# Optimization experiments

Hardware: AMD Instinct MI355X
Metric: run time of the kernel (lower is better)

Reference implementation:

```python
import jax, jax.numpy as jnp
import numpy as np
from functools import partial

PERPLEXITY = 30.0
TOL = 1e-05
K = int(3 * PERPLEXITY)  # neighbors kept after dropping self
N_CAT = 8
N_TRIES = 50


def setup_inputs() -> dict:
    key = jax.random.key(0)
    k1, k2 = jax.random.split(key)
    x = jax.random.normal(k1, (8192, 64), dtype=jnp.float32)
    batch_id = jax.random.randint(k2, (8192,), 0, N_CAT, dtype=jnp.int32)
    return {"x": x, "batch_id": batch_id}


def _knn(x):
    # squared Euclidean pairwise distances [N, N]
    sq = jnp.sum(x * x, axis=-1)
    d2 = sq[:, None] + sq[None, :] - 2.0 * (x @ x.T)
    d2 = jnp.maximum(d2, 0.0)
    neg, idx = jax.lax.top_k(-d2, K + 1)  # nearest K+1 incl. self
    dist = jnp.sqrt(jnp.maximum(-neg[:, 1:], 0.0))  # drop self -> [N, K] Euclidean
    return dist, idx[:, 1:]


def _hbeta(dist, beta):
    # dist: [N, K], beta: [N] -> entropy H [N], normalized P [N, K]
    P = jnp.exp(-dist * beta[:, None])
    Psum = jnp.sum(P, axis=1)
    safe = Psum > 0
    Psafe = jnp.where(safe, Psum, 1.0)
    H = jnp.where(safe, jnp.log(Psafe) + beta * jnp.sum(dist * P, axis=1) / Psafe, 0.0)
    Pn = jnp.where(safe[:, None], P / Psafe[:, None], 0.0)
    return H, Pn


def _beta_search(dist):
    N = dist.shape[0]
    logU = jnp.log(jnp.float32(PERPLEXITY))
    beta = jnp.ones((N,), dist.dtype)
    bmin = jnp.full((N,), -jnp.inf, dist.dtype)
    bmax = jnp.full((N,), jnp.inf, dist.dtype)
    H, P = _hbeta(dist, beta)
    Hdiff = H - logU

    def step(carry, _):
        beta, bmin, bmax, H, P, Hdiff = carry
        done = jnp.abs(Hdiff) < TOL
        pos = Hdiff > 0
        nbmin = jnp.where(pos, beta, bmin)
        nbmax = jnp.where(pos, bmax, beta)
        b_up = jnp.where(jnp.isfinite(bmax), (beta + bmax) * 0.5, beta * 2.0)
        b_dn = jnp.where(jnp.isfinite(bmin), (beta + bmin) * 0.5, beta * 0.5)
        nbeta = jnp.where(pos, b_up, b_dn)
        beta2 = jnp.where(done, beta, nbeta)
        bmin2 = jnp.where(done, bmin, nbmin)
        bmax2 = jnp.where(done, bmax, nbmax)
        Hn, Pn = _hbeta(dist, beta2)
        H2 = jnp.where(done, H, Hn)
        P2 = jnp.where(done[:, None], P, Pn)
        return (beta2, bmin2, bmax2, H2, P2, H2 - logU), None

    (beta, bmin, bmax, H, P, Hdiff), _ = jax.lax.scan(
        step, (beta, bmin, bmax, H, P, Hdiff), None, length=N_TRIES)
    return H, P


@jax.jit
def reference(x, batch_id):
    dist, idx = _knn(x)                      # [N, K], [N, K]
    H, P = _beta_search(dist)                # [N], [N, K]
    nbr_labels = batch_id[idx]               # [N, K]
    onehot = (nbr_labels[:, :, None] == jnp.arange(N_CAT)[None, None, :]).astype(P.dtype)
    contrib = jnp.einsum('nk,nkc->nc', P, onehot)   # per-category prob mass
    simpson = jnp.sum(contrib * contrib, axis=-1) + jnp.where(H == 0, -1.0, 0.0)
    return 1.0 / simpson
```

## Files before the change

### kernel.cpp

```cpp
#include <hip/hip_runtime.h>
#include <math.h>
#include <float.h>

#define N 8192
#define D 64
#define NK 90
#define NK1 (NK + 1)
#define BMR 32
#define NWAVE 16
#define BCOL (NWAVE * 32)
#define NSTEP (N / BCOL)
#define NBIN 512
#define CAP 192
#define QS 3

typedef __attribute__((ext_vector_type(8))) short short8v;
typedef __attribute__((ext_vector_type(16))) float f32x16;

__device__ __forceinline__ unsigned short f2bf(float f) {
    unsigned u = __float_as_uint(f);
    unsigned r = (u + 0x7FFFu + ((u >> 16) & 1u)) >> 16;
    return (unsigned short)r;
}
__device__ __forceinline__ float bf2f(unsigned short h) {
    return __uint_as_float(((unsigned)h) << 16);
}

__global__ void k_prep(const float* __restrict__ x, unsigned short* __restrict__ xhi,
                       unsigned short* __restrict__ xlo, float* __restrict__ sq,
                       int* __restrict__ maxbits) {
    const int r = blockIdx.x * 256 + threadIdx.x;
    const float4* p = (const float4*)(x + (size_t)r * D);
    ushort4* ph = (ushort4*)(xhi + (size_t)r * D);
    ushort4* pl = (ushort4*)(xlo + (size_t)r * D);
    float s = 0.f;
#pragma unroll
    for (int q = 0; q < D / 4; ++q) {
        float4 v = p[q];
        s += v.x * v.x + v.y * v.y + v.z * v.z + v.w * v.w;
        ushort4 hh, ll;
        hh.x = f2bf(v.x); ll.x = f2bf(v.x - bf2f(hh.x));
        hh.y = f2bf(v.y); ll.y = f2bf(v.y - bf2f(hh.y));
        hh.z = f2bf(v.z); ll.z = f2bf(v.z - bf2f(hh.z));
        hh.w = f2bf(v.w); ll.w = f2bf(v.w - bf2f(hh.w));
        ph[q] = hh; pl[q] = ll;
    }
    sq[r] = s;
    float m = s;
    for (int o = 32; o > 0; o >>= 1) m = fmaxf(m, __shfl_xor(m, o, 64));
    if ((threadIdx.x & 63) == 0) atomicMax(maxbits, __float_as_int(m));
}

__device__ __forceinline__ void wave_select(float* __restrict__ bv,
                                            unsigned short* __restrict__ bi,
                                            int n, unsigned short selfid) {
    const int lane = threadIdx.x & 63;
    const unsigned long long lt = (1ull << lane) - 1ull;
    float fv[QS]; unsigned short fi[QS]; unsigned uv[QS]; bool va[QS];
#pragma unroll
    for (int q = 0; q < QS; ++q) {
        int e = lane + 64 * q;
        bool inb = e < n;
        fv[q] = inb ? bv[e] : 0.f;
        fi[q] = inb ? bi[e] : (unsigned short)0;
        va[q] = inb && (fi[q] != selfid);
        uv[q] = __float_as_uint(fv[q]);
    }
    unsigned Tlo = 0u, Thi = 0x7F800000u;
    while (Thi - Tlo > 1u) {
        unsigned Tm = Tlo + ((Thi - Tlo) >> 1);
        int c = 0;
#pragma unroll
        for (int q = 0; q < QS; ++q)
            c += __popcll(__ballot(va[q] && uv[q] <= Tm));
        if (c >= NK) Thi = Tm; else Tlo = Tm;
    }
    int base = 0;
#pragma unroll
    for (int q = 0; q < QS; ++q) {
        bool p = va[q] && uv[q] < Thi;
        unsigned long long m = __ballot(p);
        if (p) { int pos = base + __popcll(m & lt); bv[pos] = fv[q]; bi[pos] = fi[q]; }
        base += __popcll(m);
    }
    const int c1 = base;
    const int room = NK - c1;
    int tb = 0;
#pragma unroll
    for (int q = 0; q < QS; ++q) {
        bool p = va[q] && uv[q] == Thi;
        unsigned long long m = __ballot(p);
        if (p) {
            int o = tb + __popcll(m & lt);
            if (o < room) { bv[c1 + o] = fv[q]; bi[c1 + o] = fi[q]; }
        }
        tb += __popcll(m);
    }
}

__global__ __launch_bounds__(1024) void k_knn(const unsigned short* __restrict__ xhi,
                                              const unsigned short* __restrict__ xlo,
                                              const float* __restrict__ sq,
                                              const int* __restrict__ maxbits,
                                              float* __restrict__ odist,
                                              int* __restrict__ oidx) {
    __shared__ int hist[BMR][NBIN];
    __shared__ float bufv[BMR][CAP];
    __shared__ unsigned short bufi[BMR][CAP];
    __shared__ int cnt[BMR];
    __shared__ float bsf[BMR];

    const int tid = threadIdx.x;
    const int lane = tid & 63;
    const int h = lane >> 5;
    const int wv = tid >> 6;
    const int row0 = blockIdx.x * BMR;

    for (int e = tid; e < BMR * NBIN; e += 1024) ((int*)hist)[e] = 0;
    if (tid < BMR) cnt[tid] = 0;

    const float hi = 4.0f * __int_as_float(maxbits[0]) + 1.0f;
    const float scale = (float)NBIN / hi;
    const float inv_scale = hi / (float)NBIN;
    const float ns = -2.0f * scale;

    short8v ahi[4], alo[4];
    {
        const size_t abase = (size_t)(row0 + (lane & 31)) * D + 8 * h;
#pragma unroll
        for (int ks = 0; ks < 4; ++ks) {
            ahi[ks] = *(const short8v*)(xhi + abase + ks * 16);
            alo[ks] = *(const short8v*)(xlo + abase + ks * 16);
        }
    }
    float sia_s[4][4];
#pragma unroll
    for (int q = 0; q < 4; ++q) {
        float4 t = *(const float4*)(sq + row0 + 8 * q + 4 * h);
        sia_s[q][0] = t.x * scale; sia_s[q][1] = t.y * scale;
        sia_s[q][2] = t.z * scale; sia_s[q][3] = t.w * scale;
    }
    __syncthreads();

    for (int s = 0; s < NSTEP; ++s) {
        const int gj = s * BCOL + wv * 32 + (lane & 31);
        const float sjs = sq[gj] * scale;
        f32x16 acc;
#pragma unroll
        for (int i = 0; i < 16; ++i) acc[i] = 0.f;
        const unsigned short* bh = xhi + (size_t)gj * D + 8 * h;
        const unsigned short* bl = xlo + (size_t)gj * D + 8 * h;
#pragma unroll
        for (int ks = 0; ks < 4; ++ks) {
            short8v bhiv = *(const short8v*)(bh + ks * 16);
            short8v blov = *(const short8v*)(bl + ks * 16);
            acc = __builtin_amdgcn_mfma_f32_32x32x16_bf16(ahi[ks], bhiv, acc, 0, 0, 0);
            acc = __builtin_amdgcn_mfma_f32_32x32x16_bf16(ahi[ks], blov, acc, 0, 0, 0);
            acc = __builtin_amdgcn_mfma_f32_32x32x16_bf16(alo[ks], bhiv, acc, 0, 0, 0);
        }
#pragma unroll
        for (int q = 0; q < 4; ++q)
#pragma unroll
            for (int j = 0; j < 4; ++j) {
                const int reg = 4 * q + j;
                const int rl = 8 * q + 4 * h + j;
                const float binf = fmaf(ns, acc[reg], sia_s[q][j] + sjs);
                const int bin = (int)fminf(fmaxf(binf, 0.f), 511.0f);
                atomicAdd(&hist[rl][bin], 1);
            }
    }
    __syncthreads();

#pragma unroll 1
    for (int rr = 0; rr < 2; ++rr) {
        const int r = wv * 2 + rr;
        int pc[8]; int ssum = 0;
#pragma unroll
        for (int b = 0; b < 8; ++b) { pc[b] = hist[r][lane * 8 + b]; ssum += pc[b]; }
        int incl = ssum;
        for (int o = 1; o < 64; o <<= 1) {
            int t = __shfl_up(incl, o, 64);
            if (lane >= o) incl += t;
        }
        const int excl = incl - ssum;
        const bool has = (excl < NK1) && (incl >= NK1);
        const unsigned long long m = __ballot(has);
        const int src = __ffsll((unsigned long long)m) - 1;
        int bsel = NBIN - 1;
        if (has) {
            int c = excl;
#pragma unroll
            for (int b = 0; b < 8; ++b) {
                c += pc[b];
                if (c >= NK1) { bsel = lane * 8 + b; break; }
            }
        }
        bsel = __shfl(bsel, src, 64);
        if (lane == 0) bsf[r] = (float)(bsel + 1);
    }
    __syncthreads();

    float bsr[4][4];
#pragma unroll
    for (int q = 0; q < 4; ++q) {
        float4 t = *(const float4*)(&bsf[8 * q + 4 * h]);
        bsr[q][0] = t.x; bsr[q][1] = t.y; bsr[q][2] = t.z; bsr[q][3] = t.w;
    }

    for (int s = 0; s < NSTEP; ++s) {
        const int gj = s * BCOL + wv * 32 + (lane & 31);
        const float sjs = sq[gj] * scale;
        f32x16 acc;
#pragma unroll
        for (int i = 0; i < 16; ++i) acc[i] = 0.f;
        const unsigned short* bh = xhi + (size_t)gj * D + 8 * h;
        const unsigned short* bl = xlo + (size_t)gj * D + 8 * h;
#pragma unroll
        for (int ks = 0; ks < 4; ++ks) {
            short8v bhiv = *(const short8v*)(bh + ks * 16);
            short8v blov = *(const short8v*)(bl + ks * 16);
            acc = __builtin_amdgcn_mfma_f32_32x32x16_bf16(ahi[ks], bhiv, acc, 0, 0, 0);
            acc = __builtin_amdgcn_mfma_f32_32x32x16_bf16(ahi[ks], blov, acc, 0, 0, 0);
            acc = __builtin_amdgcn_mfma_f32_32x32x16_bf16(alo[ks], bhiv, acc, 0, 0, 0);
        }
#pragma unroll
        for (int q = 0; q < 4; ++q)
#pragma unroll
            for (int j = 0; j < 4; ++j) {
                const int reg = 4 * q + j;
                const int rl = 8 * q + 4 * h + j;
                const float binf = fmaf(ns, acc[reg], sia_s[q][j] + sjs);
                const bool pred = binf < bsr[q][j];
                const unsigned long long mm = __ballot(pred);
                if (mm) {
                    const unsigned mh = (unsigned)(mm >> (h * 32));
                    int base = 0;
                    if ((lane & 31) == 0) base = atomicAdd(&cnt[rl], __popc(mh));
                    base = __shfl(base, 0, 32);
                    if (pred) {
                        const int pos = base + __popc(mh & ((1u << (lane & 31)) - 1u));
                        if (pos < CAP) {
                            bufv[rl][pos] = binf * inv_scale;
                            bufi[rl][pos] = (unsigned short)gj;
                        }
                    }
                }
            }
    }
    __syncthreads();

#pragma unroll 1
    for (int rr = 0; rr < 2; ++rr) {
        const int r = wv * 2 + rr;
        int n = cnt[r]; n = n < CAP ? n : CAP;
        wave_select(bufv[r], bufi[r], n, (unsigned short)(row0 + r));
    }
    __syncthreads();

    for (int e = tid; e < BMR * NK; e += 1024) {
        int r = e / NK, k = e - r * NK;
        odist[(row0 + r) * NK + k] = sqrtf(fmaxf(bufv[r][k], 0.f));
        oidx[(row0 + r) * NK + k] = (int)bufi[r][k];
    }
}

__global__ __launch_bounds__(256) void k_lisi(const float* __restrict__ dist,
                                              const int* __restrict__ idx,
                                              const int* __restrict__ batch,
                                              float* __restrict__ out) {
    const int wave = threadIdx.x >> 6;
    const int lane = threadIdx.x & 63;
    const int row = blockIdx.x * 4 + wave;

    const float logU = 3.4011974f;

    const float d0 = dist[row * NK + lane];
    const int i0 = idx[row * NK + lane];
    const bool v1 = lane < (NK - 64);
    const float d1 = v1 ? dist[row * NK + 64 + lane] : 0.f;
    const int i1 = v1 ? idx[row * NK + 64 + lane] : 0;
    const int l0 = batch[i0];
    const int l1 = v1 ? batch[i1] : -1;

    float beta = 1.f, bmin = -INFINITY, bmax = INFINITY;
    float P0, P1, S, H;

    auto hbeta = [&](float b) {
        P0 = __expf(-d0 * b);
        P1 = v1 ? __expf(-d1 * b) : 0.f;
        float s = P0 + P1;
        float w = d0 * P0 + (v1 ? d1 * P1 : 0.f);
        for (int o = 32; o > 0; o >>= 1) {
            s += __shfl_xor(s, o, 64);
            w += __shfl_xor(w, o, 64);
        }
        S = s;
        H = (S > 0.f) ? (__logf(S) + b * w / S) : 0.f;
    };

    hbeta(beta);
    float Hdiff = H - logU;
    for (int it = 0; it < 50; ++it) {
        if (fabsf(Hdiff) < 1e-5f) break;
        if (Hdiff > 0.f) {
            bmin = beta;
            beta = isinf(bmax) ? beta * 2.f : 0.5f * (beta + bmax);
        } else {
            bmax = beta;
            beta = isinf(bmin) ? beta * 0.5f : 0.5f * (beta + bmin);
        }
        hbeta(beta);
        Hdiff = H - logU;
    }

    const float Pn0 = (S > 0.f) ? P0 / S : 0.f;
    const float Pn1 = (S > 0.f && v1) ? P1 / S : 0.f;

    float simpson = 0.f;
#pragma unroll
    for (int c = 0; c < 8; ++c) {
        float v = (l0 == c ? Pn0 : 0.f) + (l1 == c ? Pn1 : 0.f);
        for (int o = 32; o > 0; o >>= 1) v += __shfl_xor(v, o, 64);
        simpson += v * v;
    }
    if (H == 0.f) simpson -= 1.f;
    if (lane == 0) out[row] = 1.f / simpson;
}

extern "C" void kernel_launch(void* const* d_in, const int* in_sizes, int n_in,
                              void* d_out, int out_size, void* d_ws, size_t ws_size,
                              hipStream_t stream) {
    const float* x = (const float*)d_in[0];
    const int* batch = (const int*)d_in[1];
    float* out = (float*)d_out;

    float* sq = (float*)d_ws;
    int* maxbits = (int*)(sq + N);
    unsigned short* xhi = (unsigned short*)(maxbits + 4);
    unsigned short* xlo = xhi + (size_t)N * D;
    float* dist = (float*)(xlo + (size_t)N * D);
    int* idx = (int*)(dist + (size_t)N * NK);

    k_prep<<<N / 256, 256, 0, stream>>>(x, xhi, xlo, sq, maxbits);
    k_knn<<<N / BMR, 1024, 0, stream>>>(xhi, xlo, sq, maxbits, dist, idx);
    k_lisi<<<N / 4, 256, 0, stream>>>(dist, idx, batch, out);
}
```

Measured before the change: 228.7 us.

## Split KNN into histogram/collect kernels over column halves and fuse selection with LISI

The monolithic KNN kernel becomes two kernels, a histogram pass and a candidate-collect pass. Each runs on twice as many blocks because every row band is split into two column halves, which raises occupancy across the CUs. Histograms go to global memory, and candidates are appended through global atomics. Selection moves into the LISI kernel so the dist/idx round trip disappears. The histogram drops to 256 bins and the candidate cap rises to 256. This adds extra global traffic, an extra launch, and global atomics, and coarser bins may admit more candidates.

```diff
diff --git a/kernel.cpp b/kernel.cpp
--- a/kernel.cpp
+++ b/kernel.cpp
@@ -7,12 +7,14 @@
 #define NK 90
 #define NK1 (NK + 1)
 #define BMR 32
+#define NBAND (N / BMR)
+#define HCOL (N / 2)
 #define NWAVE 16
 #define BCOL (NWAVE * 32)
-#define NSTEP (N / BCOL)
-#define NBIN 512
-#define CAP 192
-#define QS 3
+#define NSTEP (HCOL / BCOL)
+#define NBIN 256
+#define CAP 256
+#define QS 4
 
 typedef __attribute__((ext_vector_type(8))) short short8v;
 typedef __attribute__((ext_vector_type(16))) float f32x16;
@@ -28,7 +30,7 @@
 
 __global__ void k_prep(const float* __restrict__ x, unsigned short* __restrict__ xhi,
                        unsigned short* __restrict__ xlo, float* __restrict__ sq,
-                       int* __restrict__ maxbits) {
+                       int* __restrict__ maxbits, int* __restrict__ gcnt) {
     const int r = blockIdx.x * 256 + threadIdx.x;
     const float4* p = (const float4*)(x + (size_t)r * D);
     ushort4* ph = (ushort4*)(xhi + (size_t)r * D);
@@ -46,137 +48,118 @@
         ph[q] = hh; pl[q] = ll;
     }
     sq[r] = s;
+    gcnt[r] = 0;
     float m = s;
     for (int o = 32; o > 0; o >>= 1) m = fmaxf(m, __shfl_xor(m, o, 64));
     if ((threadIdx.x & 63) == 0) atomicMax(maxbits, __float_as_int(m));
 }
 
-__device__ __forceinline__ void wave_select(float* __restrict__ bv,
-                                            unsigned short* __restrict__ bi,
-                                            int n, unsigned short selfid) {
-    const int lane = threadIdx.x & 63;
-    const unsigned long long lt = (1ull << lane) - 1ull;
-    float fv[QS]; unsigned short fi[QS]; unsigned uv[QS]; bool va[QS];
-#pragma unroll
-    for (int q = 0; q < QS; ++q) {
-        int e = lane + 64 * q;
-        bool inb = e < n;
-        fv[q] = inb ? bv[e] : 0.f;
-        fi[q] = inb ? bi[e] : (unsigned short)0;
-        va[q] = inb && (fi[q] != selfid);
-        uv[q] = __float_as_uint(fv[q]);
-    }
-    unsigned Tlo = 0u, Thi = 0x7F800000u;
-    while (Thi - Tlo > 1u) {
-        unsigned Tm = Tlo + ((Thi - Tlo) >> 1);
-        int c = 0;
-#pragma unroll
-        for (int q = 0; q < QS; ++q)
-            c += __popcll(__ballot(va[q] && uv[q] <= Tm));
-        if (c >= NK) Thi = Tm; else Tlo = Tm;
-    }
-    int base = 0;
-#pragma unroll
-    for (int q = 0; q < QS; ++q) {
-        bool p = va[q] && uv[q] < Thi;
-        unsigned long long m = __ballot(p);
-        if (p) { int pos = base + __popcll(m & lt); bv[pos] = fv[q]; bi[pos] = fi[q]; }
-        base += __popcll(m);
-    }
-    const int c1 = base;
-    const int room = NK - c1;
-    int tb = 0;
-#pragma unroll
-    for (int q = 0; q < QS; ++q) {
-        bool p = va[q] && uv[q] == Thi;
-        unsigned long long m = __ballot(p);
-        if (p) {
-            int o = tb + __popcll(m & lt);
-            if (o < room) { bv[c1 + o] = fv[q]; bi[c1 + o] = fi[q]; }
-        }
-        tb += __popcll(m);
-    }
-}
-
-__global__ __launch_bounds__(1024) void k_knn(const unsigned short* __restrict__ xhi,
-                                              const unsigned short* __restrict__ xlo,
-                                              const float* __restrict__ sq,
-                                              const int* __restrict__ maxbits,
-                                              float* __restrict__ odist,
-                                              int* __restrict__ oidx) {
+__device__ __forceinline__ f32x16 dot_acc(const unsigned short* __restrict__ xhi,
+                                          const unsigned short* __restrict__ xlo,
+                                          const short8v* ahi, const short8v* alo,
+                                          int gj, int h) {
+    f32x16 acc;
+#pragma unroll
+    for (int i = 0; i < 16; ++i) acc[i] = 0.f;
+    const unsigned short* bh = xhi + (size_t)gj * D + 8 * h;
+    const unsigned short* bl = xlo + (size_t)gj * D + 8 * h;
+#pragma unroll
+    for (int ks = 0; ks < 4; ++ks) {
+        short8v bhiv = *(const short8v*)(bh + ks * 16);
+        short8v blov = *(const short8v*)(bl + ks * 16);
+        acc = __builtin_amdgcn_mfma_f32_32x32x16_bf16(ahi[ks], bhiv, acc, 0, 0, 0);
+        acc = __builtin_amdgcn_mfma_f32_32x32x16_bf16(ahi[ks], blov, acc, 0, 0, 0);
+        acc = __builtin_amdgcn_mfma_f32_32x32x16_bf16(alo[ks], bhiv, acc, 0, 0, 0);
+    }
+    return acc;
+}
+
+__global__ __launch_bounds__(1024) void k_hist(const unsigned short* __restrict__ xhi,
+                                               const unsigned short* __restrict__ xlo,
+                                               const float* __restrict__ sq,
+                                               const int* __restrict__ maxbits,
+                                               unsigned short* __restrict__ ghist) {
     __shared__ int hist[BMR][NBIN];
-    __shared__ float bufv[BMR][CAP];
-    __shared__ unsigned short bufi[BMR][CAP];
-    __shared__ int cnt[BMR];
-    __shared__ float bsf[BMR];
 
     const int tid = threadIdx.x;
     const int lane = tid & 63;
     const int h = lane >> 5;
     const int wv = tid >> 6;
-    const int row0 = blockIdx.x * BMR;
+    const int band = blockIdx.x >> 1;
+    const int colbase = (blockIdx.x & 1) * HCOL;
+    const int row0 = band * BMR;
 
     for (int e = tid; e < BMR * NBIN; e += 1024) ((int*)hist)[e] = 0;
-    if (tid < BMR) cnt[tid] = 0;
+
+    const float hi = 4.0f * __int_as_float(maxbits[0]) + 1.0f;
+    const float scale = (float)NBIN / hi;
+    const float ns = -2.0f * scale;
+
+    short8v ahi_[4], alo_[4];
+    const size_t abase = (size_t)(row0 + (lane & 31)) * D + 8 * h;
+#pragma unroll
+    for (int ks = 0; ks < 4; ++ks) {
+        ahi_[ks] = *(const short8v*)(xhi + abase + ks * 16);
+        alo_[ks] = *(const short8v*)(xlo + abase + ks * 16);
+    }
+    float sia_s[4][4];
+#pragma unroll
+    for (int q = 0; q < 4; ++q) {
+        float4 t = *(const float4*)(sq + row0 + 8 * q + 4 * h);
+        sia_s[q][0] = t.x * scale; sia_s[q][1] = t.y * scale;
+        sia_s[q][2] = t.z * scale; sia_s[q][3] = t.w * scale;
+    }
+    __syncthreads();
+
+    for (int s = 0; s < NSTEP; ++s) {
+        const int gj = colbase + s * BCOL + wv * 32 + (lane & 31);
+        const float sjs = sq[gj] * scale;
+        f32x16 acc = dot_acc(xhi, xlo, ahi_, alo_, gj, h);
+#pragma unroll
+        for (int q = 0; q < 4; ++q)
+#pragma unroll
+            for (int j = 0; j < 4; ++j) {
+                const float binf = fmaf(ns, acc[4 * q + j], sia_s[q][j] + sjs);
+                const int bin = (int)fminf(fmaxf(binf, 0.f), (float)(NBIN - 1));
+                atomicAdd(&hist[8 * q + 4 * h + j][bin], 1);
+            }
+    }
+    __syncthreads();
+
+    unsigned short* gdst = ghist + (size_t)blockIdx.x * BMR * NBIN;
+    for (int e = tid; e < BMR * NBIN; e += 1024) gdst[e] = (unsigned short)((const int*)hist)[e];
+}
+
+__global__ __launch_bounds__(1024) void k_collect(const unsigned short* __restrict__ xhi,
+                                                  const unsigned short* __restrict__ xlo,
+                                                  const float* __restrict__ sq,
+                                                  const int* __restrict__ maxbits,
+                                                  const unsigned short* __restrict__ ghist,
+                                                  int* __restrict__ gcnt,
+                                                  float* __restrict__ gbufv,
+                                                  unsigned short* __restrict__ gbufi) {
+    __shared__ float bsf[BMR];
+
+    const int tid = threadIdx.x;
+    const int lane = tid & 63;
+    const int h = lane >> 5;
+    const int wv = tid >> 6;
+    const int band = blockIdx.x >> 1;
+    const int colbase = (blockIdx.x & 1) * HCOL;
+    const int row0 = band * BMR;
 
     const float hi = 4.0f * __int_as_float(maxbits[0]) + 1.0f;
     const float scale = (float)NBIN / hi;
     const float inv_scale = hi / (float)NBIN;
     const float ns = -2.0f * scale;
 
-    short8v ahi[4], alo[4];
-    {
-        const size_t abase = (size_t)(row0 + (lane & 31)) * D + 8 * h;
-#pragma unroll
-        for (int ks = 0; ks < 4; ++ks) {
-            ahi[ks] = *(const short8v*)(xhi + abase + ks * 16);
-            alo[ks] = *(const short8v*)(xlo + abase + ks * 16);
-        }
-    }
-    float sia_s[4][4];
-#pragma unroll
-    for (int q = 0; q < 4; ++q) {
-        float4 t = *(const float4*)(sq + row0 + 8 * q + 4 * h);
-        sia_s[q][0] = t.x * scale; sia_s[q][1] = t.y * scale;
-        sia_s[q][2] = t.z * scale; sia_s[q][3] = t.w * scale;
-    }
-    __syncthreads();
-
-    for (int s = 0; s < NSTEP; ++s) {
-        const int gj = s * BCOL + wv * 32 + (lane & 31);
-        const float sjs = sq[gj] * scale;
-        f32x16 acc;
-#pragma unroll
-        for (int i = 0; i < 16; ++i) acc[i] = 0.f;
-        const unsigned short* bh = xhi + (size_t)gj * D + 8 * h;
-        const unsigned short* bl = xlo + (size_t)gj * D + 8 * h;
-#pragma unroll
-        for (int ks = 0; ks < 4; ++ks) {
-            short8v bhiv = *(const short8v*)(bh + ks * 16);
-            short8v blov = *(const short8v*)(bl + ks * 16);
-            acc = __builtin_amdgcn_mfma_f32_32x32x16_bf16(ahi[ks], bhiv, acc, 0, 0, 0);
-            acc = __builtin_amdgcn_mfma_f32_32x32x16_bf16(ahi[ks], blov, acc, 0, 0, 0);
-            acc = __builtin_amdgcn_mfma_f32_32x32x16_bf16(alo[ks], bhiv, acc, 0, 0, 0);
-        }
-#pragma unroll
-        for (int q = 0; q < 4; ++q)
-#pragma unroll
-            for (int j = 0; j < 4; ++j) {
-                const int reg = 4 * q + j;
-                const int rl = 8 * q + 4 * h + j;
-                const float binf = fmaf(ns, acc[reg], sia_s[q][j] + sjs);
-                const int bin = (int)fminf(fmaxf(binf, 0.f), 511.0f);
-                atomicAdd(&hist[rl][bin], 1);
-            }
-    }
-    __syncthreads();
-
 #pragma unroll 1
     for (int rr = 0; rr < 2; ++rr) {
         const int r = wv * 2 + rr;
-        int pc[8]; int ssum = 0;
-#pragma unroll
-        for (int b = 0; b < 8; ++b) { pc[b] = hist[r][lane * 8 + b]; ssum += pc[b]; }
+        const ushort4 h0 = *(const ushort4*)(ghist + ((size_t)(band * 2 + 0) * BMR + r) * NBIN + lane * 4);
+        const ushort4 h1 = *(const ushort4*)(ghist + ((size_t)(band * 2 + 1) * BMR + r) * NBIN + lane * 4);
+        int pc[4] = {h0.x + h1.x, h0.y + h1.y, h0.z + h1.z, h0.w + h1.w};
+        const int ssum = pc[0] + pc[1] + pc[2] + pc[3];
         int incl = ssum;
         for (int o = 1; o < 64; o <<= 1) {
             int t = __shfl_up(incl, o, 64);
@@ -190,13 +173,28 @@
         if (has) {
             int c = excl;
 #pragma unroll
-            for (int b = 0; b < 8; ++b) {
+            for (int b = 0; b < 4; ++b) {
                 c += pc[b];
-                if (c >= NK1) { bsel = lane * 8 + b; break; }
+                if (c >= NK1) { bsel = lane * 4 + b; break; }
             }
         }
         bsel = __shfl(bsel, src, 64);
         if (lane == 0) bsf[r] = (float)(bsel + 1);
+    }
+
+    short8v ahi_[4], alo_[4];
+    const size_t abase = (size_t)(row0 + (lane & 31)) * D + 8 * h;
+#pragma unroll
+    for (int ks = 0; ks < 4; ++ks) {
+        ahi_[ks] = *(const short8v*)(xhi + abase + ks * 16);
+        alo_[ks] = *(const short8v*)(xlo + abase + ks * 16);
+    }
+    float sia_s[4][4];
+#pragma unroll
+    for (int q = 0; q < 4; ++q) {
+        float4 t = *(const float4*)(sq + row0 + 8 * q + 4 * h);
+        sia_s[q][0] = t.x * scale; sia_s[q][1] = t.y * scale;
+        sia_s[q][2] = t.z * scale; sia_s[q][3] = t.w * scale;
     }
     __syncthreads();
 
@@ -208,77 +206,98 @@
     }
 
     for (int s = 0; s < NSTEP; ++s) {
-        const int gj = s * BCOL + wv * 32 + (lane & 31);
+        const int gj = colbase + s * BCOL + wv * 32 + (lane & 31);
         const float sjs = sq[gj] * scale;
-        f32x16 acc;
-#pragma unroll
-        for (int i = 0; i < 16; ++i) acc[i] = 0.f;
-        const unsigned short* bh = xhi + (size_t)gj * D + 8 * h;
-        const unsigned short* bl = xlo + (size_t)gj * D + 8 * h;
-#pragma unroll
-        for (int ks = 0; ks < 4; ++ks) {
-            short8v bhiv = *(const short8v*)(bh + ks * 16);
-            short8v blov = *(const short8v*)(bl + ks * 16);
-            acc = __builtin_amdgcn_mfma_f32_32x32x16_bf16(ahi[ks], bhiv, acc, 0, 0, 0);
-            acc = __builtin_amdgcn_mfma_f32_32x32x16_bf16(ahi[ks], blov, acc, 0, 0, 0);
-            acc = __builtin_amdgcn_mfma_f32_32x32x16_bf16(alo[ks], bhiv, acc, 0, 0, 0);
-        }
+        f32x16 acc = dot_acc(xhi, xlo, ahi_, alo_, gj, h);
 #pragma unroll
         for (int q = 0; q < 4; ++q)
 #pragma unroll
             for (int j = 0; j < 4; ++j) {
-                const int reg = 4 * q + j;
                 const int rl = 8 * q + 4 * h + j;
-                const float binf = fmaf(ns, acc[reg], sia_s[q][j] + sjs);
+                const float binf = fmaf(ns, acc[4 * q + j], sia_s[q][j] + sjs);
                 const bool pred = binf < bsr[q][j];
                 const unsigned long long mm = __ballot(pred);
                 if (mm) {
                     const unsigned mh = (unsigned)(mm >> (h * 32));
                     int base = 0;
-                    if ((lane & 31) == 0) base = atomicAdd(&cnt[rl], __popc(mh));
+                    if ((lane & 31) == 0) base = atomicAdd(&gcnt[row0 + rl], __popc(mh));
                     base = __shfl(base, 0, 32);
                     if (pred) {
                         const int pos = base + __popc(mh & ((1u << (lane & 31)) - 1u));
                         if (pos < CAP) {
-                            bufv[rl][pos] = binf * inv_scale;
-                            bufi[rl][pos] = (unsigned short)gj;
+                            gbufv[(size_t)(row0 + rl) * CAP + pos] = binf * inv_scale;
+                            gbufi[(size_t)(row0 + rl) * CAP + pos] = (unsigned short)gj;
                         }
                     }
                 }
             }
     }
-    __syncthreads();
-
-#pragma unroll 1
-    for (int rr = 0; rr < 2; ++rr) {
-        const int r = wv * 2 + rr;
-        int n = cnt[r]; n = n < CAP ? n : CAP;
-        wave_select(bufv[r], bufi[r], n, (unsigned short)(row0 + r));
-    }
-    __syncthreads();
-
-    for (int e = tid; e < BMR * NK; e += 1024) {
-        int r = e / NK, k = e - r * NK;
-        odist[(row0 + r) * NK + k] = sqrtf(fmaxf(bufv[r][k], 0.f));
-        oidx[(row0 + r) * NK + k] = (int)bufi[r][k];
-    }
-}
-
-__global__ __launch_bounds__(256) void k_lisi(const float* __restrict__ dist,
-                                              const int* __restrict__ idx,
-                                              const int* __restrict__ batch,
-                                              float* __restrict__ out) {
-    const int wave = threadIdx.x >> 6;
+}
+
+__global__ __launch_bounds__(1024) void k_sel_lisi(const float* __restrict__ gbufv,
+                                                   const unsigned short* __restrict__ gbufi,
+                                                   const int* __restrict__ gcnt,
+                                                   const int* __restrict__ batch,
+                                                   float* __restrict__ out) {
+    __shared__ float scrv[NWAVE][96];
+    __shared__ unsigned short scri[NWAVE][96];
+
     const int lane = threadIdx.x & 63;
-    const int row = blockIdx.x * 4 + wave;
+    const int w = threadIdx.x >> 6;
+    const int row = blockIdx.x * NWAVE + w;
+    const unsigned long long lt = (1ull << lane) - 1ull;
+
+    int n = gcnt[row]; n = n < CAP ? n : CAP;
+    const float* bv = gbufv + (size_t)row * CAP;
+    const unsigned short* bi = gbufi + (size_t)row * CAP;
+
+    float fv[QS]; unsigned short fi[QS]; unsigned uv[QS]; bool va[QS];
+#pragma unroll
+    for (int q = 0; q < QS; ++q) {
+        int e = lane + 64 * q;
+        bool inb = e < n;
+        fv[q] = inb ? bv[e] : 0.f;
+        fi[q] = inb ? bi[e] : (unsigned short)0;
+        va[q] = inb && (fi[q] != (unsigned short)row);
+        uv[q] = __float_as_uint(fv[q]);
+    }
+    unsigned Tlo = 0u, Thi = 0x7F800000u;
+    while (Thi - Tlo > 1u) {
+        unsigned Tm = Tlo + ((Thi - Tlo) >> 1);
+        int c = 0;
+#pragma unroll
+        for (int q = 0; q < QS; ++q)
+            c += __popcll(__ballot(va[q] && uv[q] <= Tm));
+        if (c >= NK) Thi = Tm; else Tlo = Tm;
+    }
+    int base = 0;
+#pragma unroll
+    for (int q = 0; q < QS; ++q) {
+        bool p = va[q] && uv[q] < Thi;
+        unsigned long long m = __ballot(p);
+        if (p) { int pos = base + __popcll(m & lt); scrv[w][pos] = fv[q]; scri[w][pos] = fi[q]; }
+        base += __popcll(m);
+    }
+    const int c1 = base;
+    const int room = NK - c1;
+    int tb = 0;
+#pragma unroll
+    for (int q = 0; q < QS; ++q) {
+        bool p = va[q] && uv[q] == Thi;
+        unsigned long long m = __ballot(p);
+        if (p) {
+            int o = tb + __popcll(m & lt);
+            if (o < room) { scrv[w][c1 + o] = fv[q]; scri[w][c1 + o] = fi[q]; }
+        }
+        tb += __popcll(m);
+    }
 
     const float logU = 3.4011974f;
-
-    const float d0 = dist[row * NK + lane];
-    const int i0 = idx[row * NK + lane];
+    const float d0 = sqrtf(fmaxf(scrv[w][lane], 0.f));
+    const int i0 = scri[w][lane];
     const bool v1 = lane < (NK - 64);
-    const float d1 = v1 ? dist[row * NK + 64 + lane] : 0.f;
-    const int i1 = v1 ? idx[row * NK + 64 + lane] : 0;
+    const float d1 = v1 ? sqrtf(fmaxf(scrv[w][64 + lane], 0.f)) : 0.f;
+    const int i1 = v1 ? scri[w][64 + lane] : 0;
     const int l0 = batch[i0];
     const int l1 = v1 ? batch[i1] : -1;
 
@@ -289,13 +308,13 @@
         P0 = __expf(-d0 * b);
         P1 = v1 ? __expf(-d1 * b) : 0.f;
         float s = P0 + P1;
-        float w = d0 * P0 + (v1 ? d1 * P1 : 0.f);
+        float ww = d0 * P0 + (v1 ? d1 * P1 : 0.f);
         for (int o = 32; o > 0; o >>= 1) {
             s += __shfl_xor(s, o, 64);
-            w += __shfl_xor(w, o, 64);
+            ww += __shfl_xor(ww, o, 64);
         }
         S = s;
-        H = (S > 0.f) ? (__logf(S) + b * w / S) : 0.f;
+        H = (S > 0.f) ? (__logf(S) + b * ww / S) : 0.f;
     };
 
     hbeta(beta);
@@ -336,12 +355,15 @@
 
     float* sq = (float*)d_ws;
     int* maxbits = (int*)(sq + N);
-    unsigned short* xhi = (unsigned short*)(maxbits + 4);
+    int* gcnt = maxbits + 4;
+    unsigned short* xhi = (unsigned short*)(gcnt + N);
     unsigned short* xlo = xhi + (size_t)N * D;
-    float* dist = (float*)(xlo + (size_t)N * D);
-    int* idx = (int*)(dist + (size_t)N * NK);
-
-    k_prep<<<N / 256, 256, 0, stream>>>(x, xhi, xlo, sq, maxbits);
-    k_knn<<<N / BMR, 1024, 0, stream>>>(xhi, xlo, sq, maxbits, dist, idx);
-    k_lisi<<<N / 4, 256, 0, stream>>>(dist, idx, batch, out);
-}
+    unsigned short* ghist = xlo + (size_t)N * D;
+    float* gbufv = (float*)(ghist + (size_t)2 * NBAND * BMR * NBIN);
+    unsigned short* gbufi = (unsigned short*)(gbufv + (size_t)N * CAP);
+
+    k_prep<<<N / 256, 256, 0, stream>>>(x, xhi, xlo, sq, maxbits, gcnt);
+    k_hist<<<2 * NBAND, 1024, 0, stream>>>(xhi, xlo, sq, maxbits, ghist);
+    k_collect<<<2 * NBAND, 1024, 0, stream>>>(xhi, xlo, sq, maxbits, ghist, gcnt, gbufv, gbufi);
+    k_sel_lisi<<<N / NWAVE, 1024, 0, stream>>>(gbufv, gbufi, gcnt, batch, out);
+}
```

Result: slower. 327.1 us (+43.0%).
